# Kernel tuning notes

Hardware: AMD Instinct MI355X
Metric: run time of the kernel (lower is better)

The kernel has to match this reference:

```python
import jax, jax.numpy as jnp
import numpy as np

B, CIN, COUT, H, W = 64, 2048, 32, 14, 14
REP = 1024


def setup_inputs() -> dict:
    key = jax.random.key(0)
    ks = jax.random.split(key, 7)
    x = jax.random.normal(ks[0], (B, CIN, H, W), dtype=jnp.float32)
    conv_w = jax.random.normal(ks[1], (COUT, CIN, 3, 3), dtype=jnp.float32) * (1.0 / np.sqrt(CIN * 9))
    conv_b = jax.random.normal(ks[2], (COUT,), dtype=jnp.float32) * 0.01
    w6 = jax.random.normal(ks[3], (REP, CIN * COUT), dtype=jnp.float32) * (1.0 / np.sqrt(CIN * COUT))
    b6 = jax.random.normal(ks[4], (REP,), dtype=jnp.float32) * 0.01
    w7 = jax.random.normal(ks[5], (REP, REP), dtype=jnp.float32) * (1.0 / np.sqrt(REP))
    b7 = jax.random.normal(ks[6], (REP,), dtype=jnp.float32) * 0.01
    return {"x": x, "conv_w": conv_w, "conv_b": conv_b,
            "w6": w6, "b6": b6, "w7": w7, "b7": b7}


def reference(x, conv_w, conv_b, w6, b6, w7, b7):
    # attention_map = Conv2d(in->out, k=3, s=1, p=1)(x)  -> [B, COUT, H, W]
    am = jax.lax.conv_general_dilated(
        x, conv_w, window_strides=(1, 1), padding=((1, 1), (1, 1)),
        dimension_numbers=("NCHW", "OIHW", "NCHW"))
    am = am + conv_b[None, :, None, None]
    # outer product am[:,None]*x[:,:,None] followed by AdaptiveAvgPool2d(1)
    # == mean over HW of the product: [B, CIN, COUT]
    hw = x.shape[2] * x.shape[3]
    pooled = jnp.einsum("bihw,bohw->bio", x, am) / hw
    feat = pooled.reshape(pooled.shape[0], -1)          # [B, CIN*COUT]
    h6 = jax.nn.relu(feat @ w6.T + b6)                  # [B, REP]
    out = jax.nn.relu(h6 @ w7.T + b7)                   # [B, REP]
    return out
```

## Files before the change

### kernel.cpp

```cpp
#include <hip/hip_runtime.h>
#include <hip/hip_bf16.h>

#define B_   64
#define CIN  2048
#define COUT 32
#define P    196
#define PPAD 224
#define REP  1024
#define K1   (CIN*COUT)

typedef float  f32x4  __attribute__((ext_vector_type(4)));
typedef __bf16 bf16x8 __attribute__((ext_vector_type(8)));
typedef __bf16 bf16x4 __attribute__((ext_vector_type(4)));

#define OFF_W2     0
#define OFF_AM     1310720
#define OFF_POOLED 3145728
#define OFF_S1     11534336
#define OFF_H6B    28311552
#define OFF_S2     28442624

static __device__ __forceinline__ f32x4 mfma16(bf16x8 a, bf16x8 b, f32x4 c) {
  return __builtin_amdgcn_mfma_f32_16x16x32_bf16(a, b, c, 0, 0, 0);
}

__global__ __launch_bounds__(256)
void prep_w2(const float* __restrict__ cw, __bf16* __restrict__ W2) {
  const int blk = blockIdx.x;
  const int o = blk >> 3, cc = blk & 7;
  const int cin = cc * 256 + threadIdx.x;
  const float* src = cw + ((size_t)o * CIN + cin) * 9;
  #pragma unroll
  for (int d = 0; d < 9; d++)
    W2[((size_t)d * COUT + o) * CIN + cin] = (__bf16)src[d];
}

#define ICW 72
__global__ __launch_bounds__(448)
void conv_kernel(const float* __restrict__ x, const __bf16* __restrict__ W2,
                 float* __restrict__ am) {
  __shared__ __bf16 XT[256 * ICW];

  const int ksl = blockIdx.x;
  const int b   = blockIdx.y;
  const int t   = threadIdx.x;
  const int wv  = t >> 6;
  const int lane = t & 63;
  const int q = lane >> 4, ln = lane & 15;
  const float* xb = x + (size_t)b * CIN * P;
  const int kbase = ksl * 256;

  int  rb[2];  bool valid[2];  int pix[2];
  #pragma unroll
  for (int nt = 0; nt < 2; nt++) {
    const int pt = wv * 32 + nt * 16 + ln;
    pix[nt] = pt;  valid[nt] = (pt < P);
    const int pr = valid[nt] ? pt : 0;
    const int h = pr / 14, w = pr - (pr / 14) * 14;
    rb[nt] = (h + 1) * 16 + (w + 1);
  }
  f32x4 acc[2][2];
  #pragma unroll
  for (int m = 0; m < 2; m++)
    #pragma unroll
    for (int n = 0; n < 2; n++) { f32x4 z = {0.f,0.f,0.f,0.f}; acc[m][n] = z; }

  for (int row = t; row < 256; row += 448) {
    const int hh = row >> 4, ww = row & 15;
    if (hh == 0 || hh == 15 || ww == 0 || ww == 15) {
      #pragma unroll
      for (int g = 0; g < 8; g++) {
        bf16x8 z = {};
        *(bf16x8*)&XT[row * ICW + g * 8] = z;
      }
    }
  }

  for (int sub = 0; sub < 4; sub++) {
    const int i0 = kbase + sub * 64;
    __syncthreads();
    for (int u = t; u < 1568; u += 448) {
      const int g = u / 196, p = u - g * 196;
      const int h = p / 14, w = p - (p / 14) * 14;
      bf16x8 v;
      #pragma unroll
      for (int j = 0; j < 8; j++)
        v[j] = (__bf16)xb[(size_t)(i0 + g * 8 + j) * P + p];
      *(bf16x8*)&XT[((h + 1) * 16 + (w + 1)) * ICW + g * 8] = v;
    }
    __syncthreads();

    #pragma unroll
    for (int ks2 = 0; ks2 < 2; ks2++) {
      const int kg  = i0 + ks2 * 32 + q * 8;
      const int off = (ks2 * 4 + q) * 8;
      #pragma unroll
      for (int d = 0; d < 9; d++) {
        const int dy = d / 3, dx = d - (d / 3) * 3;
        const int delta = (dy - 1) * 16 + (dx - 1);
        bf16x8 a0 = *(const bf16x8*)&W2[(size_t)(d * COUT + ln) * CIN + kg];
        bf16x8 a1 = *(const bf16x8*)&W2[(size_t)(d * COUT + 16 + ln) * CIN + kg];
        #pragma unroll
        for (int nt = 0; nt < 2; nt++) {
          bf16x8 bf = *(const bf16x8*)&XT[(rb[nt] + delta) * ICW + off];
          acc[0][nt] = mfma16(a0, bf, acc[0][nt]);
          acc[1][nt] = mfma16(a1, bf, acc[1][nt]);
        }
      }
    }
  }

  #pragma unroll
  for (int mt = 0; mt < 2; mt++)
    #pragma unroll
    for (int nt = 0; nt < 2; nt++)
      if (valid[nt]) {
        #pragma unroll
        for (int r = 0; r < 4; r++) {
          const int o = mt * 16 + q * 4 + r;
          atomicAdd(&am[((size_t)b * COUT + o) * PPAD + pix[nt]], acc[mt][nt][r]);
        }
      }
}

__global__ __launch_bounds__(256)
void pooled_kernel(const float* __restrict__ x, const float* __restrict__ amp,
                   const float* __restrict__ cb, __bf16* __restrict__ pooled) {
  const int b  = blockIdx.y;
  const int ig = blockIdx.x;
  const int t  = threadIdx.x;
  const int wv = t >> 6;
  const int lane = t & 63;
  const int q = lane >> 4, ln = lane & 15;
  const int ibase = ig * 128 + wv * 32;

  f32x4 acc[2][2];
  #pragma unroll
  for (int a = 0; a < 2; a++)
    #pragma unroll
    for (int c = 0; c < 2; c++) { f32x4 z = {0.f,0.f,0.f,0.f}; acc[a][c] = z; }

  const float* amb = amp + (size_t)b * COUT * PPAD;
  const float* xb  = x + (size_t)b * CIN * P;
  const float cbv[2] = { cb[ln], cb[16 + ln] };

  for (int kc = 0; kc < 7; kc++) {
    const int k0 = kc * 32 + q * 8;
    bf16x8 af[2];
    #pragma unroll
    for (int o2 = 0; o2 < 2; o2++) {
      const float* src = &amb[(size_t)(o2 * 16 + ln) * PPAD + k0];
      f32x4 v0 = *(const f32x4*)src;
      f32x4 v1 = *(const f32x4*)(src + 4);
      bf16x8 a;
      #pragma unroll
      for (int j = 0; j < 4; j++) { a[j] = (__bf16)(v0[j] + cbv[o2]); a[4 + j] = (__bf16)(v1[j] + cbv[o2]); }
      af[o2] = a;
    }
    #pragma unroll
    for (int it = 0; it < 2; it++) {
      const int i = ibase + it * 16 + ln;
      bf16x8 bfr;
      if (kc < 6) {
        const float* src = &xb[(size_t)i * P + k0];
        f32x4 v0 = *(const f32x4*)src;
        f32x4 v1 = *(const f32x4*)(src + 4);
        #pragma unroll
        for (int j = 0; j < 4; j++) { bfr[j] = (__bf16)v0[j]; bfr[4 + j] = (__bf16)v1[j]; }
      } else {
        #pragma unroll
        for (int j = 0; j < 8; j++) {
          const int p = k0 + j;
          bfr[j] = (p < P) ? (__bf16)xb[(size_t)i * P + p] : (__bf16)0.f;
        }
      }
      acc[0][it] = mfma16(af[0], bfr, acc[0][it]);
      acc[1][it] = mfma16(af[1], bfr, acc[1][it]);
    }
  }

  const float sc = 1.0f / 196.0f;
  #pragma unroll
  for (int o2 = 0; o2 < 2; o2++)
    #pragma unroll
    for (int it = 0; it < 2; it++) {
      const int i = ibase + it * 16 + ln;
      bf16x4 vv;
      #pragma unroll
      for (int r = 0; r < 4; r++) vv[r] = (__bf16)(acc[o2][it][r] * sc);
      *(bf16x4*)&pooled[(size_t)b * K1 + (size_t)i * COUT + o2 * 16 + q * 4] = vv;
    }
}

__global__ __launch_bounds__(256)
void gemm1_kernel(const __bf16* __restrict__ pooled, const float* __restrict__ w6,
                  float* __restrict__ S1) {
  const int nb = blockIdx.x, ks = blockIdx.y;
  const int t = threadIdx.x;
  const int wv = t >> 6;
  const int lane = t & 63;
  const int q = lane >> 4, ln = lane & 15;
  const int n0 = nb * 64 + wv * 16;
  const int kbase = ks * 1024;

  f32x4 acc[4];
  #pragma unroll
  for (int a = 0; a < 4; a++) { f32x4 z = {0.f,0.f,0.f,0.f}; acc[a] = z; }

  #pragma unroll 2
  for (int kc = 0; kc < 32; kc++) {
    const int k0 = kbase + kc * 32 + q * 8;
    const float* src = &w6[(size_t)(n0 + ln) * K1 + k0];
    f32x4 v0 = *(const f32x4*)src;
    f32x4 v1 = *(const f32x4*)(src + 4);
    bf16x8 bfr;
    #pragma unroll
    for (int j = 0; j < 4; j++) { bfr[j] = (__bf16)v0[j]; bfr[4 + j] = (__bf16)v1[j]; }
    #pragma unroll
    for (int mi = 0; mi < 4; mi++) {
      bf16x8 af = *(const bf16x8*)&pooled[(size_t)(mi * 16 + ln) * K1 + k0];
      acc[mi] = mfma16(af, bfr, acc[mi]);
    }
  }
  #pragma unroll
  for (int mi = 0; mi < 4; mi++)
    #pragma unroll
    for (int r = 0; r < 4; r++)
      S1[(size_t)ks * (B_ * REP) + (size_t)(mi * 16 + q * 4 + r) * REP + n0 + ln] = acc[mi][r];
}

__global__ __launch_bounds__(256)
void reduce1_kernel(const float* __restrict__ S1, const float* __restrict__ b6,
                    __bf16* __restrict__ h6b) {
  const int idx = blockIdx.x * 256 + threadIdx.x;
  float s = 0.f;
  #pragma unroll 8
  for (int ks = 0; ks < 64; ks++) s += S1[(size_t)ks * (B_ * REP) + idx];
  h6b[idx] = (__bf16)fmaxf(s + b6[idx & (REP - 1)], 0.f);
}

__global__ __launch_bounds__(256)
void gemm2_kernel(const __bf16* __restrict__ h6b, const float* __restrict__ w7,
                  float* __restrict__ S2) {
  const int nb = blockIdx.x, ks = blockIdx.y;
  const int t = threadIdx.x;
  const int wv = t >> 6;
  const int lane = t & 63;
  const int q = lane >> 4, ln = lane & 15;
  const int n0 = nb * 64 + wv * 16;
  const int k0 = ks * 32 + q * 8;

  const float* src = &w7[(size_t)(n0 + ln) * REP + k0];
  f32x4 v0 = *(const f32x4*)src;
  f32x4 v1 = *(const f32x4*)(src + 4);
  bf16x8 bfr;
  #pragma unroll
  for (int j = 0; j < 4; j++) { bfr[j] = (__bf16)v0[j]; bfr[4 + j] = (__bf16)v1[j]; }

  f32x4 acc[4];
  #pragma unroll
  for (int mi = 0; mi < 4; mi++) {
    f32x4 z = {0.f,0.f,0.f,0.f};
    bf16x8 af = *(const bf16x8*)&h6b[(size_t)(mi * 16 + ln) * REP + k0];
    acc[mi] = mfma16(af, bfr, z);
  }
  #pragma unroll
  for (int mi = 0; mi < 4; mi++)
    #pragma unroll
    for (int r = 0; r < 4; r++)
      S2[(size_t)ks * (B_ * REP) + (size_t)(mi * 16 + q * 4 + r) * REP + n0 + ln] = acc[mi][r];
}

__global__ __launch_bounds__(256)
void reduce2_kernel(const float* __restrict__ S2, const float* __restrict__ b7,
                    float* __restrict__ out) {
  const int idx = blockIdx.x * 256 + threadIdx.x;
  float s = 0.f;
  #pragma unroll 8
  for (int ks = 0; ks < 32; ks++) s += S2[(size_t)ks * (B_ * REP) + idx];
  out[idx] = fmaxf(s + b7[idx & (REP - 1)], 0.f);
}

extern "C" void kernel_launch(void* const* d_in, const int* in_sizes, int n_in,
                              void* d_out, int out_size, void* d_ws, size_t ws_size,
                              hipStream_t stream) {
  const float* x   = (const float*)d_in[0];
  const float* cw  = (const float*)d_in[1];
  const float* cb  = (const float*)d_in[2];
  const float* w6  = (const float*)d_in[3];
  const float* b6  = (const float*)d_in[4];
  const float* w7  = (const float*)d_in[5];
  const float* b7  = (const float*)d_in[6];
  float* out = (float*)d_out;

  char* ws = (char*)d_ws;
  __bf16* W2     = (__bf16*)(ws + OFF_W2);
  float*  am     = (float*)(ws + OFF_AM);
  __bf16* pooled = (__bf16*)(ws + OFF_POOLED);
  float*  S1     = (float*)(ws + OFF_S1);
  __bf16* h6b    = (__bf16*)(ws + OFF_H6B);
  float*  S2     = (float*)(ws + OFF_S2);

  hipMemsetAsync(am, 0, (size_t)B_ * COUT * PPAD * 4, stream);
  prep_w2       <<<256,          256, 0, stream>>>(cw, W2);
  conv_kernel   <<<dim3(8, 64),  448, 0, stream>>>(x, W2, am);
  pooled_kernel <<<dim3(16, 64), 256, 0, stream>>>(x, am, cb, pooled);
  gemm1_kernel  <<<dim3(16, 64), 256, 0, stream>>>(pooled, w6, S1);
  reduce1_kernel<<<256,          256, 0, stream>>>(S1, b6, h6b);
  gemm2_kernel  <<<dim3(16, 32), 256, 0, stream>>>(h6b, w7, S2);
  reduce2_kernel<<<256,          256, 0, stream>>>(S2, b7, out);
}
```

Before: 580.1 us.

## Fuse all stages into one cooperative persistent kernel with grid syncs

```diff
diff --git a/kernel.cpp b/kernel.cpp
--- a/kernel.cpp
+++ b/kernel.cpp
@@ -1,5 +1,8 @@
 #include <hip/hip_runtime.h>
 #include <hip/hip_bf16.h>
+#include <hip/hip_cooperative_groups.h>
+
+namespace cg = cooperative_groups;
 
 #define B_   64
 #define CIN  2048
@@ -24,261 +27,264 @@
   return __builtin_amdgcn_mfma_f32_16x16x32_bf16(a, b, c, 0, 0, 0);
 }
 
-__global__ __launch_bounds__(256)
-void prep_w2(const float* __restrict__ cw, __bf16* __restrict__ W2) {
-  const int blk = blockIdx.x;
-  const int o = blk >> 3, cc = blk & 7;
-  const int cin = cc * 256 + threadIdx.x;
-  const float* src = cw + ((size_t)o * CIN + cin) * 9;
-  #pragma unroll
-  for (int d = 0; d < 9; d++)
-    W2[((size_t)d * COUT + o) * CIN + cin] = (__bf16)src[d];
-}
-
 #define ICW 72
-__global__ __launch_bounds__(448)
-void conv_kernel(const float* __restrict__ x, const __bf16* __restrict__ W2,
-                 float* __restrict__ am) {
+
+__global__ __launch_bounds__(256, 2)
+void mega_kernel(const float* __restrict__ x,  const float* __restrict__ cw,
+                 const float* __restrict__ cb, const float* __restrict__ w6,
+                 const float* __restrict__ b6, const float* __restrict__ w7,
+                 const float* __restrict__ b7,
+                 __bf16* __restrict__ W2, float* __restrict__ am,
+                 __bf16* __restrict__ pooled, float* __restrict__ S1,
+                 __bf16* __restrict__ h6b, float* __restrict__ S2,
+                 float* __restrict__ out) {
   __shared__ __bf16 XT[256 * ICW];
-
-  const int ksl = blockIdx.x;
-  const int b   = blockIdx.y;
-  const int t   = threadIdx.x;
-  const int wv  = t >> 6;
+  cg::grid_group grid = cg::this_grid();
+
+  const int blk  = blockIdx.x;
+  const int t    = threadIdx.x;
+  const int wv   = t >> 6;
   const int lane = t & 63;
-  const int q = lane >> 4, ln = lane & 15;
-  const float* xb = x + (size_t)b * CIN * P;
-  const int kbase = ksl * 256;
-
-  int  rb[2];  bool valid[2];  int pix[2];
-  #pragma unroll
-  for (int nt = 0; nt < 2; nt++) {
-    const int pt = wv * 32 + nt * 16 + ln;
-    pix[nt] = pt;  valid[nt] = (pt < P);
-    const int pr = valid[nt] ? pt : 0;
-    const int h = pr / 14, w = pr - (pr / 14) * 14;
-    rb[nt] = (h + 1) * 16 + (w + 1);
-  }
-  f32x4 acc[2][2];
-  #pragma unroll
-  for (int m = 0; m < 2; m++)
-    #pragma unroll
-    for (int n = 0; n < 2; n++) { f32x4 z = {0.f,0.f,0.f,0.f}; acc[m][n] = z; }
-
-  for (int row = t; row < 256; row += 448) {
-    const int hh = row >> 4, ww = row & 15;
-    if (hh == 0 || hh == 15 || ww == 0 || ww == 15) {
-      #pragma unroll
-      for (int g = 0; g < 8; g++) {
-        bf16x8 z = {};
-        *(bf16x8*)&XT[row * ICW + g * 8] = z;
-      }
-    }
-  }
-
-  for (int sub = 0; sub < 4; sub++) {
-    const int i0 = kbase + sub * 64;
-    __syncthreads();
-    for (int u = t; u < 1568; u += 448) {
-      const int g = u / 196, p = u - g * 196;
-      const int h = p / 14, w = p - (p / 14) * 14;
-      bf16x8 v;
-      #pragma unroll
-      for (int j = 0; j < 8; j++)
-        v[j] = (__bf16)xb[(size_t)(i0 + g * 8 + j) * P + p];
-      *(bf16x8*)&XT[((h + 1) * 16 + (w + 1)) * ICW + g * 8] = v;
-    }
-    __syncthreads();
-
-    #pragma unroll
-    for (int ks2 = 0; ks2 < 2; ks2++) {
-      const int kg  = i0 + ks2 * 32 + q * 8;
-      const int off = (ks2 * 4 + q) * 8;
-      #pragma unroll
-      for (int d = 0; d < 9; d++) {
-        const int dy = d / 3, dx = d - (d / 3) * 3;
-        const int delta = (dy - 1) * 16 + (dx - 1);
-        bf16x8 a0 = *(const bf16x8*)&W2[(size_t)(d * COUT + ln) * CIN + kg];
-        bf16x8 a1 = *(const bf16x8*)&W2[(size_t)(d * COUT + 16 + ln) * CIN + kg];
-        #pragma unroll
-        for (int nt = 0; nt < 2; nt++) {
-          bf16x8 bf = *(const bf16x8*)&XT[(rb[nt] + delta) * ICW + off];
-          acc[0][nt] = mfma16(a0, bf, acc[0][nt]);
-          acc[1][nt] = mfma16(a1, bf, acc[1][nt]);
+  const int q    = lane >> 4, ln = lane & 15;
+
+  if (blk < 256) {
+    const int o = blk >> 3, cc = blk & 7;
+    const int cin = cc * 256 + t;
+    const float* src = cw + ((size_t)o * CIN + cin) * 9;
+    #pragma unroll
+    for (int d = 0; d < 9; d++)
+      W2[((size_t)d * COUT + o) * CIN + cin] = (__bf16)src[d];
+  } else {
+    #pragma unroll
+    for (int k = 0; k < 7; k++)
+      am[(size_t)(blk - 256) * 256 + t + (size_t)k * 65536] = 0.f;
+  }
+  grid.sync();
+
+  {
+    const int ksl = blk & 7;
+    const int bb  = blk >> 3;
+    const float* xb = x + (size_t)bb * CIN * P;
+    const int kbase = ksl * 256;
+
+    int rb[4]; bool valid[4]; int pix[4]; bool tv[4];
+    #pragma unroll
+    for (int nt = 0; nt < 4; nt++) {
+      const int tile = wv * 4 + nt;
+      const int pt = tile * 16 + ln;
+      tv[nt]    = (tile <= 12);
+      valid[nt] = (pt < P);
+      pix[nt]   = pt;
+      const int pr = valid[nt] ? pt : 0;
+      const int h = pr / 14, w = pr - (pr / 14) * 14;
+      rb[nt] = (h + 1) * 16 + (w + 1);
+    }
+    f32x4 acc[2][4];
+    #pragma unroll
+    for (int m = 0; m < 2; m++)
+      #pragma unroll
+      for (int n = 0; n < 4; n++) { f32x4 z = {0.f,0.f,0.f,0.f}; acc[m][n] = z; }
+
+    {
+      const int row = t, hh = row >> 4, ww = row & 15;
+      if (hh == 0 || hh == 15 || ww == 0 || ww == 15) {
+        #pragma unroll
+        for (int g = 0; g < 8; g++) { bf16x8 z = {}; *(bf16x8*)&XT[row * ICW + g * 8] = z; }
+      }
+    }
+
+    for (int sub = 0; sub < 4; sub++) {
+      const int i0 = kbase + sub * 64;
+      __syncthreads();
+      for (int u = t; u < 1568; u += 256) {
+        const int g = u / 196, p = u - g * 196;
+        const int h = p / 14, w = p - (p / 14) * 14;
+        bf16x8 v;
+        #pragma unroll
+        for (int j = 0; j < 8; j++)
+          v[j] = (__bf16)xb[(size_t)(i0 + g * 8 + j) * P + p];
+        *(bf16x8*)&XT[((h + 1) * 16 + (w + 1)) * ICW + g * 8] = v;
+      }
+      __syncthreads();
+
+      #pragma unroll
+      for (int ks2 = 0; ks2 < 2; ks2++) {
+        const int kg  = i0 + ks2 * 32 + q * 8;
+        const int off = (ks2 * 4 + q) * 8;
+        #pragma unroll
+        for (int d = 0; d < 9; d++) {
+          const int dy = d / 3, dx = d - (d / 3) * 3;
+          const int delta = (dy - 1) * 16 + (dx - 1);
+          bf16x8 a0 = *(const bf16x8*)&W2[(size_t)(d * COUT + ln) * CIN + kg];
+          bf16x8 a1 = *(const bf16x8*)&W2[(size_t)(d * COUT + 16 + ln) * CIN + kg];
+          #pragma unroll
+          for (int nt = 0; nt < 4; nt++) {
+            if (tv[nt]) {
+              bf16x8 bf = *(const bf16x8*)&XT[(rb[nt] + delta) * ICW + off];
+              acc[0][nt] = mfma16(a0, bf, acc[0][nt]);
+              acc[1][nt] = mfma16(a1, bf, acc[1][nt]);
+            }
+          }
         }
       }
     }
-  }
-
-  #pragma unroll
-  for (int mt = 0; mt < 2; mt++)
-    #pragma unroll
-    for (int nt = 0; nt < 2; nt++)
-      if (valid[nt]) {
-        #pragma unroll
-        for (int r = 0; r < 4; r++) {
-          const int o = mt * 16 + q * 4 + r;
-          atomicAdd(&am[((size_t)b * COUT + o) * PPAD + pix[nt]], acc[mt][nt][r]);
+
+    #pragma unroll
+    for (int mt = 0; mt < 2; mt++)
+      #pragma unroll
+      for (int nt = 0; nt < 4; nt++)
+        if (valid[nt]) {
+          #pragma unroll
+          for (int r = 0; r < 4; r++) {
+            const int o = mt * 16 + q * 4 + r;
+            atomicAdd(&am[((size_t)bb * COUT + o) * PPAD + pix[nt]], acc[mt][nt][r]);
+          }
         }
-      }
-}
-
-__global__ __launch_bounds__(256)
-void pooled_kernel(const float* __restrict__ x, const float* __restrict__ amp,
-                   const float* __restrict__ cb, __bf16* __restrict__ pooled) {
-  const int b  = blockIdx.y;
-  const int ig = blockIdx.x;
-  const int t  = threadIdx.x;
-  const int wv = t >> 6;
-  const int lane = t & 63;
-  const int q = lane >> 4, ln = lane & 15;
-  const int ibase = ig * 128 + wv * 32;
-
-  f32x4 acc[2][2];
-  #pragma unroll
-  for (int a = 0; a < 2; a++)
-    #pragma unroll
-    for (int c = 0; c < 2; c++) { f32x4 z = {0.f,0.f,0.f,0.f}; acc[a][c] = z; }
-
-  const float* amb = amp + (size_t)b * COUT * PPAD;
-  const float* xb  = x + (size_t)b * CIN * P;
-  const float cbv[2] = { cb[ln], cb[16 + ln] };
-
-  for (int kc = 0; kc < 7; kc++) {
-    const int k0 = kc * 32 + q * 8;
-    bf16x8 af[2];
-    #pragma unroll
-    for (int o2 = 0; o2 < 2; o2++) {
-      const float* src = &amb[(size_t)(o2 * 16 + ln) * PPAD + k0];
+  }
+  grid.sync();
+
+  for (int vv = blk; vv < 1024; vv += 512) {
+    const int ig = vv & 15, bb = vv >> 4;
+    const int ibase = ig * 128 + wv * 32;
+
+    f32x4 acc[2][2];
+    #pragma unroll
+    for (int a = 0; a < 2; a++)
+      #pragma unroll
+      for (int c = 0; c < 2; c++) { f32x4 z = {0.f,0.f,0.f,0.f}; acc[a][c] = z; }
+
+    const float* amb = am + (size_t)bb * COUT * PPAD;
+    const float* xb  = x + (size_t)bb * CIN * P;
+    const float cbv[2] = { cb[ln], cb[16 + ln] };
+
+    for (int kc = 0; kc < 7; kc++) {
+      const int k0 = kc * 32 + q * 8;
+      bf16x8 af[2];
+      #pragma unroll
+      for (int o2 = 0; o2 < 2; o2++) {
+        const float* src = &amb[(size_t)(o2 * 16 + ln) * PPAD + k0];
+        f32x4 v0 = *(const f32x4*)src;
+        f32x4 v1 = *(const f32x4*)(src + 4);
+        bf16x8 a;
+        #pragma unroll
+        for (int j = 0; j < 4; j++) { a[j] = (__bf16)(v0[j] + cbv[o2]); a[4 + j] = (__bf16)(v1[j] + cbv[o2]); }
+        af[o2] = a;
+      }
+      #pragma unroll
+      for (int it = 0; it < 2; it++) {
+        const int i = ibase + it * 16 + ln;
+        bf16x8 bfr;
+        if (kc < 6) {
+          const float* src = &xb[(size_t)i * P + k0];
+          f32x4 v0 = *(const f32x4*)src;
+          f32x4 v1 = *(const f32x4*)(src + 4);
+          #pragma unroll
+          for (int j = 0; j < 4; j++) { bfr[j] = (__bf16)v0[j]; bfr[4 + j] = (__bf16)v1[j]; }
+        } else {
+          #pragma unroll
+          for (int j = 0; j < 8; j++) {
+            const int p = k0 + j;
+            bfr[j] = (p < P) ? (__bf16)xb[(size_t)i * P + p] : (__bf16)0.f;
+          }
+        }
+        acc[0][it] = mfma16(af[0], bfr, acc[0][it]);
+        acc[1][it] = mfma16(af[1], bfr, acc[1][it]);
+      }
+    }
+
+    const float sc = 1.0f / 196.0f;
+    #pragma unroll
+    for (int o2 = 0; o2 < 2; o2++)
+      #pragma unroll
+      for (int it = 0; it < 2; it++) {
+        const int i = ibase + it * 16 + ln;
+        bf16x4 vvv;
+        #pragma unroll
+        for (int r = 0; r < 4; r++) vvv[r] = (__bf16)(acc[o2][it][r] * sc);
+        *(bf16x4*)&pooled[(size_t)bb * K1 + (size_t)i * COUT + o2 * 16 + q * 4] = vvv;
+      }
+  }
+  grid.sync();
+
+  for (int vv = blk; vv < 1024; vv += 512) {
+    const int nb = vv & 15, ks = vv >> 4;
+    const int n0 = nb * 64 + wv * 16;
+    const int kbase = ks * 1024;
+
+    f32x4 acc[4];
+    #pragma unroll
+    for (int a = 0; a < 4; a++) { f32x4 z = {0.f,0.f,0.f,0.f}; acc[a] = z; }
+
+    #pragma unroll 2
+    for (int kc = 0; kc < 32; kc++) {
+      const int k0 = kbase + kc * 32 + q * 8;
+      const float* src = &w6[(size_t)(n0 + ln) * K1 + k0];
       f32x4 v0 = *(const f32x4*)src;
       f32x4 v1 = *(const f32x4*)(src + 4);
-      bf16x8 a;
-      #pragma unroll
-      for (int j = 0; j < 4; j++) { a[j] = (__bf16)(v0[j] + cbv[o2]); a[4 + j] = (__bf16)(v1[j] + cbv[o2]); }
-      af[o2] = a;
-    }
-    #pragma unroll
-    for (int it = 0; it < 2; it++) {
-      const int i = ibase + it * 16 + ln;
       bf16x8 bfr;
-      if (kc < 6) {
-        const float* src = &xb[(size_t)i * P + k0];
-        f32x4 v0 = *(const f32x4*)src;
-        f32x4 v1 = *(const f32x4*)(src + 4);
-        #pragma unroll
-        for (int j = 0; j < 4; j++) { bfr[j] = (__bf16)v0[j]; bfr[4 + j] = (__bf16)v1[j]; }
-      } else {
-        #pragma unroll
-        for (int j = 0; j < 8; j++) {
-          const int p = k0 + j;
-          bfr[j] = (p < P) ? (__bf16)xb[(size_t)i * P + p] : (__bf16)0.f;
-        }
-      }
-      acc[0][it] = mfma16(af[0], bfr, acc[0][it]);
-      acc[1][it] = mfma16(af[1], bfr, acc[1][it]);
-    }
-  }
-
-  const float sc = 1.0f / 196.0f;
-  #pragma unroll
-  for (int o2 = 0; o2 < 2; o2++)
-    #pragma unroll
-    for (int it = 0; it < 2; it++) {
-      const int i = ibase + it * 16 + ln;
-      bf16x4 vv;
-      #pragma unroll
-      for (int r = 0; r < 4; r++) vv[r] = (__bf16)(acc[o2][it][r] * sc);
-      *(bf16x4*)&pooled[(size_t)b * K1 + (size_t)i * COUT + o2 * 16 + q * 4] = vv;
-    }
-}
-
-__global__ __launch_bounds__(256)
-void gemm1_kernel(const __bf16* __restrict__ pooled, const float* __restrict__ w6,
-                  float* __restrict__ S1) {
-  const int nb = blockIdx.x, ks = blockIdx.y;
-  const int t = threadIdx.x;
-  const int wv = t >> 6;
-  const int lane = t & 63;
-  const int q = lane >> 4, ln = lane & 15;
-  const int n0 = nb * 64 + wv * 16;
-  const int kbase = ks * 1024;
-
-  f32x4 acc[4];
-  #pragma unroll
-  for (int a = 0; a < 4; a++) { f32x4 z = {0.f,0.f,0.f,0.f}; acc[a] = z; }
-
-  #pragma unroll 2
-  for (int kc = 0; kc < 32; kc++) {
-    const int k0 = kbase + kc * 32 + q * 8;
-    const float* src = &w6[(size_t)(n0 + ln) * K1 + k0];
-    f32x4 v0 = *(const f32x4*)src;
-    f32x4 v1 = *(const f32x4*)(src + 4);
-    bf16x8 bfr;
-    #pragma unroll
-    for (int j = 0; j < 4; j++) { bfr[j] = (__bf16)v0[j]; bfr[4 + j] = (__bf16)v1[j]; }
-    #pragma unroll
-    for (int mi = 0; mi < 4; mi++) {
-      bf16x8 af = *(const bf16x8*)&pooled[(size_t)(mi * 16 + ln) * K1 + k0];
-      acc[mi] = mfma16(af, bfr, acc[mi]);
-    }
-  }
-  #pragma unroll
-  for (int mi = 0; mi < 4; mi++)
-    #pragma unroll
-    for (int r = 0; r < 4; r++)
-      S1[(size_t)ks * (B_ * REP) + (size_t)(mi * 16 + q * 4 + r) * REP + n0 + ln] = acc[mi][r];
-}
-
-__global__ __launch_bounds__(256)
-void reduce1_kernel(const float* __restrict__ S1, const float* __restrict__ b6,
-                    __bf16* __restrict__ h6b) {
-  const int idx = blockIdx.x * 256 + threadIdx.x;
-  float s = 0.f;
-  #pragma unroll 8
-  for (int ks = 0; ks < 64; ks++) s += S1[(size_t)ks * (B_ * REP) + idx];
-  h6b[idx] = (__bf16)fmaxf(s + b6[idx & (REP - 1)], 0.f);
-}
-
-__global__ __launch_bounds__(256)
-void gemm2_kernel(const __bf16* __restrict__ h6b, const float* __restrict__ w7,
-                  float* __restrict__ S2) {
-  const int nb = blockIdx.x, ks = blockIdx.y;
-  const int t = threadIdx.x;
-  const int wv = t >> 6;
-  const int lane = t & 63;
-  const int q = lane >> 4, ln = lane & 15;
-  const int n0 = nb * 64 + wv * 16;
-  const int k0 = ks * 32 + q * 8;
-
-  const float* src = &w7[(size_t)(n0 + ln) * REP + k0];
-  f32x4 v0 = *(const f32x4*)src;
-  f32x4 v1 = *(const f32x4*)(src + 4);
-  bf16x8 bfr;
-  #pragma unroll
-  for (int j = 0; j < 4; j++) { bfr[j] = (__bf16)v0[j]; bfr[4 + j] = (__bf16)v1[j]; }
-
-  f32x4 acc[4];
-  #pragma unroll
-  for (int mi = 0; mi < 4; mi++) {
-    f32x4 z = {0.f,0.f,0.f,0.f};
-    bf16x8 af = *(const bf16x8*)&h6b[(size_t)(mi * 16 + ln) * REP + k0];
-    acc[mi] = mfma16(af, bfr, z);
-  }
-  #pragma unroll
-  for (int mi = 0; mi < 4; mi++)
-    #pragma unroll
-    for (int r = 0; r < 4; r++)
-      S2[(size_t)ks * (B_ * REP) + (size_t)(mi * 16 + q * 4 + r) * REP + n0 + ln] = acc[mi][r];
-}
-
-__global__ __launch_bounds__(256)
-void reduce2_kernel(const float* __restrict__ S2, const float* __restrict__ b7,
-                    float* __restrict__ out) {
-  const int idx = blockIdx.x * 256 + threadIdx.x;
-  float s = 0.f;
-  #pragma unroll 8
-  for (int ks = 0; ks < 32; ks++) s += S2[(size_t)ks * (B_ * REP) + idx];
-  out[idx] = fmaxf(s + b7[idx & (REP - 1)], 0.f);
+      #pragma unroll
+      for (int j = 0; j < 4; j++) { bfr[j] = (__bf16)v0[j]; bfr[4 + j] = (__bf16)v1[j]; }
+      #pragma unroll
+      for (int mi = 0; mi < 4; mi++) {
+        bf16x8 af = *(const bf16x8*)&pooled[(size_t)(mi * 16 + ln) * K1 + k0];
+        acc[mi] = mfma16(af, bfr, acc[mi]);
+      }
+    }
+    #pragma unroll
+    for (int mi = 0; mi < 4; mi++)
+      #pragma unroll
+      for (int r = 0; r < 4; r++)
+        S1[(size_t)ks * (B_ * REP) + (size_t)(mi * 16 + q * 4 + r) * REP + n0 + ln] = acc[mi][r];
+  }
+  grid.sync();
+
+  if (blk < 256) {
+    const int idx = blk * 256 + t;
+    float s = 0.f;
+    #pragma unroll 8
+    for (int ks = 0; ks < 64; ks++) s += S1[(size_t)ks * (B_ * REP) + idx];
+    h6b[idx] = (__bf16)fmaxf(s + b6[idx & (REP - 1)], 0.f);
+  }
+  grid.sync();
+
+  if (blk < 128) {
+    const int nb = blk & 15, ks = blk >> 4;
+    const int n0 = nb * 64 + wv * 16;
+
+    f32x4 acc[4];
+    #pragma unroll
+    for (int a = 0; a < 4; a++) { f32x4 z = {0.f,0.f,0.f,0.f}; acc[a] = z; }
+
+    #pragma unroll
+    for (int kc = 0; kc < 4; kc++) {
+      const int k0 = ks * 128 + kc * 32 + q * 8;
+      const float* src = &w7[(size_t)(n0 + ln) * REP + k0];
+      f32x4 v0 = *(const f32x4*)src;
+      f32x4 v1 = *(const f32x4*)(src + 4);
+      bf16x8 bfr;
+      #pragma unroll
+      for (int j = 0; j < 4; j++) { bfr[j] = (__bf16)v0[j]; bfr[4 + j] = (__bf16)v1[j]; }
+      #pragma unroll
+      for (int mi = 0; mi < 4; mi++) {
+        bf16x8 af = *(const bf16x8*)&h6b[(size_t)(mi * 16 + ln) * REP + k0];
+        acc[mi] = mfma16(af, bfr, acc[mi]);
+      }
+    }
+    #pragma unroll
+    for (int mi = 0; mi < 4; mi++)
+      #pragma unroll
+      for (int r = 0; r < 4; r++)
+        S2[(size_t)ks * (B_ * REP) + (size_t)(mi * 16 + q * 4 + r) * REP + n0 + ln] = acc[mi][r];
+  }
+  grid.sync();
+
+  if (blk < 256) {
+    const int idx = blk * 256 + t;
+    float s = 0.f;
+    #pragma unroll
+    for (int ks = 0; ks < 8; ks++) s += S2[(size_t)ks * (B_ * REP) + idx];
+    out[idx] = fmaxf(s + b7[idx & (REP - 1)], 0.f);
+  }
 }
 
 extern "C" void kernel_launch(void* const* d_in, const int* in_sizes, int n_in,
@@ -301,12 +307,9 @@
   __bf16* h6b    = (__bf16*)(ws + OFF_H6B);
   float*  S2     = (float*)(ws + OFF_S2);
 
-  hipMemsetAsync(am, 0, (size_t)B_ * COUT * PPAD * 4, stream);
-  prep_w2       <<<256,          256, 0, stream>>>(cw, W2);
-  conv_kernel   <<<dim3(8, 64),  448, 0, stream>>>(x, W2, am);
-  pooled_kernel <<<dim3(16, 64), 256, 0, stream>>>(x, am, cb, pooled);
-  gemm1_kernel  <<<dim3(16, 64), 256, 0, stream>>>(pooled, w6, S1);
-  reduce1_kernel<<<256,          256, 0, stream>>>(S1, b6, h6b);
-  gemm2_kernel  <<<dim3(16, 32), 256, 0, stream>>>(h6b, w7, S2);
-  reduce2_kernel<<<256,          256, 0, stream>>>(S2, b7, out);
+  void* args[] = { (void*)&x, (void*)&cw, (void*)&cb, (void*)&w6, (void*)&b6,
+                   (void*)&w7, (void*)&b7, (void*)&W2, (void*)&am, (void*)&pooled,
+                   (void*)&S1, (void*)&h6b, (void*)&S2, (void*)&out };
+  hipLaunchCooperativeKernel(reinterpret_cast<void*>(mega_kernel),
+                             dim3(512), dim3(256), args, 0, stream);
 }
```

Measured after the change: 896.5 us. 54.6% more time.

## Replace conv atomics with split-K partial buffers, prefetch x tiles, rebalance GEMM splits

Applied to the files above, without the earlier changes.

```diff
diff --git a/kernel.cpp b/kernel.cpp
--- a/kernel.cpp
+++ b/kernel.cpp
@@ -8,17 +8,19 @@
 #define PPAD 224
 #define REP  1024
 #define K1   (CIN*COUT)
+#define NSL  16
 
 typedef float  f32x4  __attribute__((ext_vector_type(4)));
 typedef __bf16 bf16x8 __attribute__((ext_vector_type(8)));
 typedef __bf16 bf16x4 __attribute__((ext_vector_type(4)));
 
 #define OFF_W2     0
-#define OFF_AM     1310720
-#define OFF_POOLED 3145728
-#define OFF_S1     11534336
-#define OFF_H6B    28311552
-#define OFF_S2     28442624
+#define OFF_AMP    1179648
+#define OFF_AMBF   30539776
+#define OFF_POOLED 31457280
+#define OFF_S1     39845888
+#define OFF_H6B    48234496
+#define OFF_S2     48365568
 
 static __device__ __forceinline__ f32x4 mfma16(bf16x8 a, bf16x8 b, f32x4 c) {
   return __builtin_amdgcn_mfma_f32_16x16x32_bf16(a, b, c, 0, 0, 0);
@@ -38,23 +40,23 @@
 #define ICW 72
 __global__ __launch_bounds__(448)
 void conv_kernel(const float* __restrict__ x, const __bf16* __restrict__ W2,
-                 float* __restrict__ am) {
+                 float* __restrict__ amp) {
   __shared__ __bf16 XT[256 * ICW];
 
   const int ksl = blockIdx.x;
-  const int b   = blockIdx.y;
+  const int bb  = blockIdx.y;
   const int t   = threadIdx.x;
   const int wv  = t >> 6;
   const int lane = t & 63;
   const int q = lane >> 4, ln = lane & 15;
-  const float* xb = x + (size_t)b * CIN * P;
-  const int kbase = ksl * 256;
-
-  int  rb[2];  bool valid[2];  int pix[2];
+  const float* xb = x + (size_t)bb * CIN * P;
+  const int kbase = ksl * 128;
+
+  int rb[2]; bool valid[2]; int pix[2];
   #pragma unroll
   for (int nt = 0; nt < 2; nt++) {
     const int pt = wv * 32 + nt * 16 + ln;
-    pix[nt] = pt;  valid[nt] = (pt < P);
+    pix[nt] = pt; valid[nt] = (pt < P);
     const int pr = valid[nt] ? pt : 0;
     const int h = pr / 14, w = pr - (pr / 14) * 14;
     rb[nt] = (h + 1) * 16 + (w + 1);
@@ -65,31 +67,57 @@
     #pragma unroll
     for (int n = 0; n < 2; n++) { f32x4 z = {0.f,0.f,0.f,0.f}; acc[m][n] = z; }
 
-  for (int row = t; row < 256; row += 448) {
-    const int hh = row >> 4, ww = row & 15;
-    if (hh == 0 || hh == 15 || ww == 0 || ww == 15) {
-      #pragma unroll
-      for (int g = 0; g < 8; g++) {
-        bf16x8 z = {};
-        *(bf16x8*)&XT[row * ICW + g * 8] = z;
-      }
-    }
-  }
-
-  for (int sub = 0; sub < 4; sub++) {
-    const int i0 = kbase + sub * 64;
-    __syncthreads();
-    for (int u = t; u < 1568; u += 448) {
+  const int nIter = (t < 224) ? 4 : 3;
+  int obase[4], dst[4];
+  #pragma unroll
+  for (int it = 0; it < 4; it++) {
+    const int u = t + 448 * it;
+    if (u < 1568) {
       const int g = u / 196, p = u - g * 196;
       const int h = p / 14, w = p - (p / 14) * 14;
+      obase[it] = (g * 8) * P + p;
+      dst[it]   = ((h + 1) * 16 + (w + 1)) * ICW + g * 8;
+    } else { obase[it] = 0; dst[it] = 0; }
+  }
+
+  bf16x8 pre[4];
+  #pragma unroll
+  for (int it = 0; it < 4; it++)
+    if (it < nIter) {
       bf16x8 v;
       #pragma unroll
       for (int j = 0; j < 8; j++)
-        v[j] = (__bf16)xb[(size_t)(i0 + g * 8 + j) * P + p];
-      *(bf16x8*)&XT[((h + 1) * 16 + (w + 1)) * ICW + g * 8] = v;
-    }
-    __syncthreads();
-
+        v[j] = (__bf16)xb[(size_t)kbase * P + obase[it] + j * P];
+      pre[it] = v;
+    }
+
+  if (t < 256) {
+    const int hh = t >> 4, ww = t & 15;
+    if (hh == 0 || hh == 15 || ww == 0 || ww == 15) {
+      #pragma unroll
+      for (int g = 0; g < 8; g++) { bf16x8 z = {}; *(bf16x8*)&XT[t * ICW + g * 8] = z; }
+    }
+  }
+
+  #pragma unroll
+  for (int it = 0; it < 4; it++)
+    if (it < nIter) *(bf16x8*)&XT[dst[it]] = pre[it];
+
+  #pragma unroll
+  for (int it = 0; it < 4; it++)
+    if (it < nIter) {
+      bf16x8 v;
+      #pragma unroll
+      for (int j = 0; j < 8; j++)
+        v[j] = (__bf16)xb[(size_t)(kbase + 64) * P + obase[it] + j * P];
+      pre[it] = v;
+    }
+
+  __syncthreads();
+
+  #pragma unroll
+  for (int sub = 0; sub < 2; sub++) {
+    const int i0 = kbase + sub * 64;
     #pragma unroll
     for (int ks2 = 0; ks2 < 2; ks2++) {
       const int kg  = i0 + ks2 * 32 + q * 8;
@@ -108,8 +136,16 @@
         }
       }
     }
-  }
-
+    if (sub == 0) {
+      __syncthreads();
+      #pragma unroll
+      for (int it = 0; it < 4; it++)
+        if (it < nIter) *(bf16x8*)&XT[dst[it]] = pre[it];
+      __syncthreads();
+    }
+  }
+
+  float* dstp = amp + (((size_t)ksl * B_ + bb) * COUT) * PPAD;
   #pragma unroll
   for (int mt = 0; mt < 2; mt++)
     #pragma unroll
@@ -118,14 +154,32 @@
         #pragma unroll
         for (int r = 0; r < 4; r++) {
           const int o = mt * 16 + q * 4 + r;
-          atomicAdd(&am[((size_t)b * COUT + o) * PPAD + pix[nt]], acc[mt][nt][r]);
+          dstp[(size_t)o * PPAD + pix[nt]] = acc[mt][nt][r];
         }
       }
 }
 
 __global__ __launch_bounds__(256)
-void pooled_kernel(const float* __restrict__ x, const float* __restrict__ amp,
-                   const float* __restrict__ cb, __bf16* __restrict__ pooled) {
+void am_final_kernel(const float* __restrict__ amp, const float* __restrict__ cb,
+                     __bf16* __restrict__ am_bf) {
+  const int NE = B_ * COUT * PPAD;
+  for (int e = blockIdx.x * 256 + threadIdx.x; e < NE; e += 448 * 256) {
+    const int row = e / PPAD;
+    const int pe  = e - row * PPAD;
+    float v = 0.f;
+    if (pe < P) {
+      float s = 0.f;
+      #pragma unroll
+      for (int sl = 0; sl < NSL; sl++) s += amp[(size_t)sl * NE + e];
+      v = s + cb[row & (COUT - 1)];
+    }
+    am_bf[e] = (__bf16)v;
+  }
+}
+
+__global__ __launch_bounds__(256)
+void pooled_kernel(const float* __restrict__ x, const __bf16* __restrict__ amb_,
+                   __bf16* __restrict__ pooled) {
   const int b  = blockIdx.y;
   const int ig = blockIdx.x;
   const int t  = threadIdx.x;
@@ -140,23 +194,16 @@
     #pragma unroll
     for (int c = 0; c < 2; c++) { f32x4 z = {0.f,0.f,0.f,0.f}; acc[a][c] = z; }
 
-  const float* amb = amp + (size_t)b * COUT * PPAD;
-  const float* xb  = x + (size_t)b * CIN * P;
-  const float cbv[2] = { cb[ln], cb[16 + ln] };
-
+  const __bf16* amb = amb_ + (size_t)b * COUT * PPAD;
+  const float*  xb  = x + (size_t)b * CIN * P;
+
+  #pragma unroll
   for (int kc = 0; kc < 7; kc++) {
     const int k0 = kc * 32 + q * 8;
     bf16x8 af[2];
     #pragma unroll
-    for (int o2 = 0; o2 < 2; o2++) {
-      const float* src = &amb[(size_t)(o2 * 16 + ln) * PPAD + k0];
-      f32x4 v0 = *(const f32x4*)src;
-      f32x4 v1 = *(const f32x4*)(src + 4);
-      bf16x8 a;
-      #pragma unroll
-      for (int j = 0; j < 4; j++) { a[j] = (__bf16)(v0[j] + cbv[o2]); a[4 + j] = (__bf16)(v1[j] + cbv[o2]); }
-      af[o2] = a;
-    }
+    for (int o2 = 0; o2 < 2; o2++)
+      af[o2] = *(const bf16x8*)&amb[(size_t)(o2 * 16 + ln) * PPAD + k0];
     #pragma unroll
     for (int it = 0; it < 2; it++) {
       const int i = ibase + it * 16 + ln;
@@ -201,14 +248,14 @@
   const int lane = t & 63;
   const int q = lane >> 4, ln = lane & 15;
   const int n0 = nb * 64 + wv * 16;
-  const int kbase = ks * 1024;
+  const int kbase = ks * 2048;
 
   f32x4 acc[4];
   #pragma unroll
   for (int a = 0; a < 4; a++) { f32x4 z = {0.f,0.f,0.f,0.f}; acc[a] = z; }
 
-  #pragma unroll 2
-  for (int kc = 0; kc < 32; kc++) {
+  #pragma unroll 4
+  for (int kc = 0; kc < 64; kc++) {
     const int k0 = kbase + kc * 32 + q * 8;
     const float* src = &w6[(size_t)(n0 + ln) * K1 + k0];
     f32x4 v0 = *(const f32x4*)src;
@@ -235,7 +282,7 @@
   const int idx = blockIdx.x * 256 + threadIdx.x;
   float s = 0.f;
   #pragma unroll 8
-  for (int ks = 0; ks < 64; ks++) s += S1[(size_t)ks * (B_ * REP) + idx];
+  for (int ks = 0; ks < 32; ks++) s += S1[(size_t)ks * (B_ * REP) + idx];
   h6b[idx] = (__bf16)fmaxf(s + b6[idx & (REP - 1)], 0.f);
 }
 
@@ -248,21 +295,25 @@
   const int lane = t & 63;
   const int q = lane >> 4, ln = lane & 15;
   const int n0 = nb * 64 + wv * 16;
-  const int k0 = ks * 32 + q * 8;
-
-  const float* src = &w7[(size_t)(n0 + ln) * REP + k0];
-  f32x4 v0 = *(const f32x4*)src;
-  f32x4 v1 = *(const f32x4*)(src + 4);
-  bf16x8 bfr;
-  #pragma unroll
-  for (int j = 0; j < 4; j++) { bfr[j] = (__bf16)v0[j]; bfr[4 + j] = (__bf16)v1[j]; }
 
   f32x4 acc[4];
   #pragma unroll
-  for (int mi = 0; mi < 4; mi++) {
-    f32x4 z = {0.f,0.f,0.f,0.f};
-    bf16x8 af = *(const bf16x8*)&h6b[(size_t)(mi * 16 + ln) * REP + k0];
-    acc[mi] = mfma16(af, bfr, z);
+  for (int a = 0; a < 4; a++) { f32x4 z = {0.f,0.f,0.f,0.f}; acc[a] = z; }
+
+  #pragma unroll
+  for (int kc = 0; kc < 4; kc++) {
+    const int k0 = ks * 128 + kc * 32 + q * 8;
+    const float* src = &w7[(size_t)(n0 + ln) * REP + k0];
+    f32x4 v0 = *(const f32x4*)src;
+    f32x4 v1 = *(const f32x4*)(src + 4);
+    bf16x8 bfr;
+    #pragma unroll
+    for (int j = 0; j < 4; j++) { bfr[j] = (__bf16)v0[j]; bfr[4 + j] = (__bf16)v1[j]; }
+    #pragma unroll
+    for (int mi = 0; mi < 4; mi++) {
+      bf16x8 af = *(const bf16x8*)&h6b[(size_t)(mi * 16 + ln) * REP + k0];
+      acc[mi] = mfma16(af, bfr, acc[mi]);
+    }
   }
   #pragma unroll
   for (int mi = 0; mi < 4; mi++)
@@ -276,8 +327,8 @@
                     float* __restrict__ out) {
   const int idx = blockIdx.x * 256 + threadIdx.x;
   float s = 0.f;
-  #pragma unroll 8
-  for (int ks = 0; ks < 32; ks++) s += S2[(size_t)ks * (B_ * REP) + idx];
+  #pragma unroll
+  for (int ks = 0; ks < 8; ks++) s += S2[(size_t)ks * (B_ * REP) + idx];
   out[idx] = fmaxf(s + b7[idx & (REP - 1)], 0.f);
 }
 
@@ -295,18 +346,19 @@
 
   char* ws = (char*)d_ws;
   __bf16* W2     = (__bf16*)(ws + OFF_W2);
-  float*  am     = (float*)(ws + OFF_AM);
+  float*  amp    = (float*)(ws + OFF_AMP);
+  __bf16* am_bf  = (__bf16*)(ws + OFF_AMBF);
   __bf16* pooled = (__bf16*)(ws + OFF_POOLED);
   float*  S1     = (float*)(ws + OFF_S1);
   __bf16* h6b    = (__bf16*)(ws + OFF_H6B);
   float*  S2     = (float*)(ws + OFF_S2);
 
-  hipMemsetAsync(am, 0, (size_t)B_ * COUT * PPAD * 4, stream);
-  prep_w2       <<<256,          256, 0, stream>>>(cw, W2);
-  conv_kernel   <<<dim3(8, 64),  448, 0, stream>>>(x, W2, am);
-  pooled_kernel <<<dim3(16, 64), 256, 0, stream>>>(x, am, cb, pooled);
-  gemm1_kernel  <<<dim3(16, 64), 256, 0, stream>>>(pooled, w6, S1);
-  reduce1_kernel<<<256,          256, 0, stream>>>(S1, b6, h6b);
-  gemm2_kernel  <<<dim3(16, 32), 256, 0, stream>>>(h6b, w7, S2);
-  reduce2_kernel<<<256,          256, 0, stream>>>(S2, b7, out);
-}
+  prep_w2        <<<256,          256, 0, stream>>>(cw, W2);
+  conv_kernel    <<<dim3(16, 64), 448, 0, stream>>>(x, W2, amp);
+  am_final_kernel<<<448,          256, 0, stream>>>(amp, cb, am_bf);
+  pooled_kernel  <<<dim3(16, 64), 256, 0, stream>>>(x, am_bf, pooled);
+  gemm1_kernel   <<<dim3(16, 32), 256, 0, stream>>>(pooled, w6, S1);
+  reduce1_kernel <<<256,          256, 0, stream>>>(S1, b6, h6b);
+  gemm2_kernel   <<<dim3(16, 8),  256, 0, stream>>>(h6b, w7, S2);
+  reduce2_kernel <<<256,          256, 0, stream>>>(S2, b7, out);
+}
```

New measurement: 572.7 us. No clear change (-1.3%).
